# Kernel optimization log

Hardware: AMD Instinct MI355X
Metric: run time of the kernel (lower is better)

## Reference

```python
import jax, jax.numpy as jnp
import numpy as np

ALPHA = 0.25
GAMMA = 2.0
EPS = 1e-8


def _lsa(cost):
    """Jonker-Volgenant shortest-augmenting-path linear sum assignment.
    Matches scipy.optimize.linear_sum_assignment for rectangular matrices."""
    cost = np.asarray(cost, dtype=np.float64)
    transposed = cost.shape[0] > cost.shape[1]
    if transposed:
        cost = cost.T
    n, m = cost.shape  # n <= m
    INF = 1e18
    u = np.zeros(n + 1)
    v = np.zeros(m + 1)
    p = np.zeros(m + 1, dtype=np.int64)   # p[j] = row (1-indexed) assigned to col j
    way = np.zeros(m + 1, dtype=np.int64)
    for i in range(1, n + 1):
        p[0] = i
        j0 = 0
        minv = np.full(m + 1, INF)
        used = np.zeros(m + 1, dtype=bool)
        while True:
            used[j0] = True
            i0 = p[j0]
            cur = cost[i0 - 1] - u[i0] - v[1:]
            free = ~used[1:]
            better = free & (cur < minv[1:])
            minv[1:][better] = cur[better]
            way[1:][better] = j0
            masked = np.where(free, minv[1:], INF)
            j1 = int(np.argmin(masked)) + 1
            delta = masked[j1 - 1]
            u[p[used]] += delta
            v[used] -= delta
            minv[1:][free] -= delta
            j0 = j1
            if p[j0] == 0:
                break
        while j0 != 0:  # augment
            j1 = way[j0]
            p[j0] = p[j1]
            j0 = j1
    row_of_col = p[1:] - 1
    cols = np.nonzero(row_of_col >= 0)[0]
    rows = row_of_col[cols]
    if transposed:
        rows, cols = cols, rows
    order = np.argsort(rows)
    return rows[order], cols[order]


def _focal_cost(p):
    """pos_cost - neg_cost for sigmoid probs p, per focal-loss matcher cost."""
    neg = (1.0 - ALPHA) * p ** GAMMA * (-jnp.log(1.0 - p + EPS))
    pos = ALPHA * (1.0 - p) ** GAMMA * (-jnp.log(p + EPS))
    return pos - neg


def _match(rec, loc, targets):
    """rec: [bs, Q, Crec] logits; loc: [bs, Q, Cloc] logits; targets: [bs, nt] int.
    Returns (src_idx, tgt_idx) each [bs, nt] (query index, target index)."""
    nt = targets.shape[1]
    cost_class = jnp.take_along_axis(_focal_cost(jax.nn.sigmoid(rec)),
                                     targets[:, None, :], axis=2)      # [bs, Q, nt]
    cost_pos = _focal_cost(jax.nn.sigmoid(loc))[:, :, :nt]             # tgt_pos = arange(nt)
    C = np.asarray(2.0 * cost_class + cost_pos)                        # [bs, Q, nt]
    src, tgt = [], []
    for b in range(C.shape[0]):  # per-batch Hungarian, as in original
        r, c = _lsa(C[b])
        src.append(r)
        tgt.append(c)
    return jnp.asarray(np.stack(src)), jnp.asarray(np.stack(tgt))


def _ce(logits, labels):
    # F.cross_entropy with mean reduction
    logp = jax.nn.log_softmax(logits, axis=-1)
    return -jnp.mean(jnp.take_along_axis(logp, labels[..., None], axis=-1))


def setup_inputs() -> dict:
    key = jax.random.key(0)
    k1, k2, k3 = jax.random.split(key, 3)
    rec = jax.random.normal(k1, (128, 107, 32, 32), dtype=jnp.float32)
    loc = jax.random.normal(k2, (128, 25, 32, 32), dtype=jnp.float32)
    targets = jax.random.randint(k3, (128, 25), 0, 107, dtype=jnp.int64)
    return {"rec": rec, "loc": loc, "targets": targets}


def reference(rec, loc, targets):
    bs, c_rec, H, W = rec.shape
    c_loc = loc.shape[1]
    nt = targets.shape[1]
    rec = jnp.transpose(rec.reshape(bs, c_rec, H * W), (0, 2, 1))  # [bs, Q, Crec]
    loc = jnp.transpose(loc.reshape(bs, c_loc, H * W), (0, 2, 1))  # [bs, Q, Cloc]
    src_idx, tgt_idx = _match(rec, loc, targets)                   # [bs, nt] each
    rec_m = jnp.take_along_axis(rec, src_idx[:, :, None], axis=1)  # [bs, nt, Crec]
    loc_m = jnp.take_along_axis(loc, src_idx[:, :, None], axis=1)  # [bs, nt, Cloc]
    cls_labels = jnp.take_along_axis(targets, tgt_idx, axis=1)     # [bs, nt]
    pos_labels = tgt_idx                                           # tgt_pos[b, j] == j
    det_rec_losses = _ce(rec_m.reshape(bs * nt, c_rec), cls_labels.reshape(-1))
    pos_losses = _ce(loc_m.reshape(bs * nt, c_loc), pos_labels.reshape(-1))
    return (det_rec_losses, pos_losses)
```

## Files before the change

kernel.cpp:

```cpp
#include <hip/hip_runtime.h>
#include <hip/hip_bf16.h>
#include <math.h>

#define BS   128
#define NT   25
#define CREC 107
#define CLOC 25
#define QN   1024
#define INFD 1e18

__device__ __forceinline__ float focal_cost_f(float x) {
    float p   = 1.0f / (1.0f + __expf(-x));
    float neg = 0.75f * p * p * (-__logf(1.0f - p + 1e-8f));
    float pos = 0.25f * (1.0f - p) * (1.0f - p) * (-__logf(p + 1e-8f));
    return pos - neg;
}

__global__ __launch_bounds__(256)
void hungarian_kernel(const float* __restrict__ rec, const float* __restrict__ loc,
                      const int* __restrict__ targets, int* __restrict__ pairq_g) {
    const int b     = blockIdx.x;
    const int tid   = threadIdx.x;
    const int wave  = tid >> 6;
    const int lane  = tid & 63;
    const int qbase = (wave << 8) + (lane << 2);

    __shared__ int    way_s[QN + 1];
    __shared__ int    p_s[QN + 1];
    __shared__ double u_s[NT + 1];
    __shared__ int    t_s[NT];
    __shared__ float  bminv_s[NT][4];
    __shared__ int    bminq_s[NT][4];
    __shared__ float  rowmin_s[NT];
    __shared__ int    rowarg_s[NT];
    __shared__ int    unassigned_s[NT];
    __shared__ int    nun_s;
    __shared__ double candv_s[4];
    __shared__ int    candj_s[4];

    for (int j = tid; j <= QN; j += 256) { p_s[j] = 0; way_s[j] = 0; }
    if (tid < NT) t_s[tid] = targets[b * NT + tid];
    __syncthreads();

    const size_t rb0 = (size_t)b * CREC * QN;
    const size_t lb0 = (size_t)b * CLOC * QN;

    {
        float4 ra = *(const float4*)(rec + rb0 + (size_t)t_s[0] * QN + qbase);
        float4 la = *(const float4*)(loc + lb0 + qbase);
        for (int r = 0; r < NT; ++r) {
            float4 rn, ln;
            if (r + 1 < NT) {
                rn = *(const float4*)(rec + rb0 + (size_t)t_s[r + 1] * QN + qbase);
                ln = *(const float4*)(loc + lb0 + (size_t)(r + 1) * QN + qbase);
            }
            float c[4];
            c[0] = 2.0f * focal_cost_f(ra.x) + focal_cost_f(la.x);
            c[1] = 2.0f * focal_cost_f(ra.y) + focal_cost_f(la.y);
            c[2] = 2.0f * focal_cost_f(ra.z) + focal_cost_f(la.z);
            c[3] = 2.0f * focal_cost_f(ra.w) + focal_cost_f(la.w);
            float bv = c[0]; int bq = qbase;
            #pragma unroll
            for (int m = 1; m < 4; ++m)
                if (c[m] < bv) { bv = c[m]; bq = qbase + m; }
            #pragma unroll
            for (int off = 32; off; off >>= 1) {
                float ov = __shfl_xor(bv, off);
                int   oq = __shfl_xor(bq, off);
                if (ov < bv || (ov == bv && oq < bq)) { bv = ov; bq = oq; }
            }
            if (lane == 0) { bminv_s[r][wave] = bv; bminq_s[r][wave] = bq; }
            ra = rn; la = ln;
        }
    }
    __syncthreads();
    if (tid < NT) {
        float bv = bminv_s[tid][0]; int bq = bminq_s[tid][0];
        #pragma unroll
        for (int w = 1; w < 4; ++w) {
            float ov = bminv_s[tid][w]; int oq = bminq_s[tid][w];
            if (ov < bv || (ov == bv && oq < bq)) { bv = ov; bq = oq; }
        }
        rowmin_s[tid] = bv; rowarg_s[tid] = bq;
    }
    __syncthreads();
    if (tid == 0) {
        nun_s = 0;
        for (int r = 0; r < NT; ++r) {
            u_s[r + 1] = (double)rowmin_s[r];
            int j = rowarg_s[r] + 1;
            if (p_s[j] == 0) p_s[j] = r + 1;
            else             unassigned_s[nun_s++] = r + 1;
        }
    }
    __syncthreads();
    const int nun = nun_s;

    double v[4] = {0.0, 0.0, 0.0, 0.0};

    for (int s = 0; s < nun; ++s) {
        const int i = unassigned_s[s];
        double minv[4] = {INFD, INFD, INFD, INFD};
        unsigned usedmask = 0;
        int j0 = 0;

        for (;;) {
            int i0;
            if (j0 == 0) {
                i0 = i;
            } else {
                int q0 = j0 - 1;
                if ((q0 >> 2) == tid) {
                    int m = q0 & 3;
                    usedmask |= 1u << m;
                    minv[m] = INFD;
                }
                i0 = p_s[j0];
            }
            const double ui0 = u_s[i0];
            const float4 r4 = *(const float4*)(rec + rb0 + (size_t)t_s[i0 - 1] * QN + qbase);
            const float4 l4 = *(const float4*)(loc + lb0 + (size_t)(i0 - 1) * QN + qbase);
            float cf[4];
            cf[0] = 2.0f * focal_cost_f(r4.x) + focal_cost_f(l4.x);
            cf[1] = 2.0f * focal_cost_f(r4.y) + focal_cost_f(l4.y);
            cf[2] = 2.0f * focal_cost_f(r4.z) + focal_cost_f(l4.z);
            cf[3] = 2.0f * focal_cost_f(r4.w) + focal_cost_f(l4.w);

            double bestv = INFD; int bestj = QN + 2;
            #pragma unroll
            for (int m = 0; m < 4; ++m) {
                if (!(usedmask & (1u << m))) {
                    const int j = qbase + m + 1;
                    double cur = (double)cf[m] - ui0 - v[m];
                    if (cur < minv[m]) { minv[m] = cur; way_s[j] = j0; }
                    double mv = minv[m];
                    if (mv < bestv || (mv == bestv && j < bestj)) { bestv = mv; bestj = j; }
                }
            }
            #pragma unroll
            for (int off = 32; off; off >>= 1) {
                double ov = __shfl_xor(bestv, off);
                int    oj = __shfl_xor(bestj, off);
                if (ov < bestv || (ov == bestv && oj < bestj)) { bestv = ov; bestj = oj; }
            }
            if (lane == 0) { candv_s[wave] = bestv; candj_s[wave] = bestj; }
            __syncthreads();
            double delta = candv_s[0]; int j1 = candj_s[0];
            #pragma unroll
            for (int w = 1; w < 4; ++w) {
                double dv = candv_s[w]; int dj = candj_s[w];
                if (dv < delta || (dv == delta && dj < j1)) { delta = dv; j1 = dj; }
            }

            #pragma unroll
            for (int m = 0; m < 4; ++m) {
                if (usedmask & (1u << m)) v[m]    -= delta;
                else                      minv[m] -= delta;
            }
            if (tid == 0) u_s[i] += delta;
            unsigned mm = usedmask;
            while (mm) {
                int m = __ffs(mm) - 1; mm &= mm - 1;
                u_s[p_s[qbase + m + 1]] += delta;
            }
            __syncthreads();

            j0 = j1;
            if (p_s[j0] == 0) break;
        }
        if (tid == 0) {
            int jj = j0;
            while (jj != 0) {
                int jn = way_s[jj];
                p_s[jj] = (jn == 0) ? i : p_s[jn];
                jj = jn;
            }
        }
        __syncthreads();
    }

    for (int j = tid + 1; j <= QN; j += 256)
        if (p_s[j] > 0) pairq_g[b * NT + (p_s[j] - 1)] = j - 1;
}

__global__ __launch_bounds__(64)
void loss_kernel(const float* __restrict__ rec, const float* __restrict__ loc,
                 const int* __restrict__ targets, const int* __restrict__ pairq_g,
                 float* __restrict__ partial) {
    const int pid  = blockIdx.x;
    const int b    = pid / NT, t = pid % NT;
    const int lane = threadIdx.x;
    const int q    = pairq_g[pid];

    const float* rb = rec + (size_t)b * CREC * QN + q;
    float x0 = (lane < CREC)      ? rb[(size_t)lane * QN]        : -1e30f;
    float x1 = (lane + 64 < CREC) ? rb[(size_t)(lane + 64) * QN] : -1e30f;
    float mx = fmaxf(x0, x1);
    #pragma unroll
    for (int off = 32; off; off >>= 1) mx = fmaxf(mx, __shfl_xor(mx, off));
    float e = 0.0f;
    if (lane < CREC)      e += expf(x0 - mx);
    if (lane + 64 < CREC) e += expf(x1 - mx);
    #pragma unroll
    for (int off = 32; off; off >>= 1) e += __shfl_xor(e, off);
    float lse = mx + logf(e);

    const float* lb = loc + (size_t)b * CLOC * QN + q;
    float y = (lane < CLOC) ? lb[(size_t)lane * QN] : -1e30f;
    float my = y;
    #pragma unroll
    for (int off = 32; off; off >>= 1) my = fmaxf(my, __shfl_xor(my, off));
    float ey = (lane < CLOC) ? expf(y - my) : 0.0f;
    #pragma unroll
    for (int off = 32; off; off >>= 1) ey += __shfl_xor(ey, off);
    float lsey = my + logf(ey);

    if (lane == 0) {
        int lab = targets[pid];
        partial[pid]           = lse  - rb[(size_t)lab * QN];
        partial[BS * NT + pid] = lsey - lb[(size_t)t * QN];
    }
}

__global__ __launch_bounds__(256)
void finalize_kernel(const float* __restrict__ partial, float* __restrict__ out) {
    const int tid = threadIdx.x;
    float s0 = 0.0f, s1 = 0.0f;
    for (int i = tid; i < BS * NT; i += 256) {
        s0 += partial[i];
        s1 += partial[BS * NT + i];
    }
    __shared__ float a0[4], a1[4];
    #pragma unroll
    for (int off = 32; off; off >>= 1) { s0 += __shfl_xor(s0, off); s1 += __shfl_xor(s1, off); }
    if ((tid & 63) == 0) { a0[tid >> 6] = s0; a1[tid >> 6] = s1; }
    __syncthreads();
    if (tid == 0) {
        out[0] = (a0[0] + a0[1] + a0[2] + a0[3]) * (1.0f / (BS * NT));
        out[1] = (a1[0] + a1[1] + a1[2] + a1[3]) * (1.0f / (BS * NT));
    }
}

extern "C" void kernel_launch(void* const* d_in, const int* in_sizes, int n_in,
                              void* d_out, int out_size, void* d_ws, size_t ws_size,
                              hipStream_t stream) {
    (void)in_sizes; (void)n_in; (void)out_size; (void)ws_size;
    const float* rec     = (const float*)d_in[0];
    const float* loc     = (const float*)d_in[1];
    const int*   targets = (const int*)d_in[2];
    float* out = (float*)d_out;

    int*   pairq_g = (int*)d_ws;
    float* partial = (float*)(pairq_g + BS * NT);

    hipLaunchKernelGGL(hungarian_kernel, dim3(BS), dim3(256), 0, stream,
                       rec, loc, targets, pairq_g);
    hipLaunchKernelGGL(loss_kernel, dim3(BS * NT), dim3(64), 0, stream,
                       rec, loc, targets, pairq_g, partial);
    hipLaunchKernelGGL(finalize_kernel, dim3(1), dim3(256), 0, stream,
                       partial, out);
}
```

Measured before the change: 167.1 us.

## Split row-min init into parallel kernel and remove per-step barrier in Dijkstra loop

Moves the initial per-row minimum computation out of the per-batch Hungarian kernel into a separate kernel launched over batch×target blocks, so that work spreads across many more workgroups. Inside the augmenting search, the dual update of u is deferred to the end of each search using a running delta sum and per-column snapshots, and candidate slots are double-buffered by parity, which removes one __syncthreads per inner iteration. The way array is re-laid out with a padded stride to spread LDS banks. The cost is an extra launch, a global round trip for the row minima, and a little more register state per thread.

```diff
diff --git a/kernel.cpp b/kernel.cpp
--- a/kernel.cpp
+++ b/kernel.cpp
@@ -8,6 +8,11 @@
 #define CLOC 25
 #define QN   1024
 #define INFD 1e18
+#define WSTR 257
+__device__ __forceinline__ int widx(int j) {
+    int q = j - 1;
+    return (q & 3) * WSTR + (q >> 2);
+}
 
 __device__ __forceinline__ float focal_cost_f(float x) {
     float p   = 1.0f / (1.0f + __expf(-x));
@@ -17,73 +22,78 @@
 }
 
 __global__ __launch_bounds__(256)
-void hungarian_kernel(const float* __restrict__ rec, const float* __restrict__ loc,
-                      const int* __restrict__ targets, int* __restrict__ pairq_g) {
+void rowmin_kernel(const float* __restrict__ rec, const float* __restrict__ loc,
+                   const int* __restrict__ targets,
+                   float* __restrict__ rowmin_g, int* __restrict__ rowarg_g) {
+    const int pid   = blockIdx.x;
+    const int b     = pid / NT, r = pid % NT;
+    const int tid   = threadIdx.x;
+    const int qbase = tid << 2;
+    const int tc    = targets[pid];
+
+    float4 r4 = *(const float4*)(rec + ((size_t)b * CREC + tc) * QN + qbase);
+    float4 l4 = *(const float4*)(loc + ((size_t)b * CLOC + r)  * QN + qbase);
+    float c[4];
+    c[0] = 2.0f * focal_cost_f(r4.x) + focal_cost_f(l4.x);
+    c[1] = 2.0f * focal_cost_f(r4.y) + focal_cost_f(l4.y);
+    c[2] = 2.0f * focal_cost_f(r4.z) + focal_cost_f(l4.z);
+    c[3] = 2.0f * focal_cost_f(r4.w) + focal_cost_f(l4.w);
+
+    float bv = c[0]; int bq = qbase;
+    #pragma unroll
+    for (int m = 1; m < 4; ++m)
+        if (c[m] < bv) { bv = c[m]; bq = qbase + m; }
+    #pragma unroll
+    for (int off = 32; off; off >>= 1) {
+        float ov = __shfl_xor(bv, off);
+        int   oq = __shfl_xor(bq, off);
+        if (ov < bv || (ov == bv && oq < bq)) { bv = ov; bq = oq; }
+    }
+    __shared__ float bmv[4];
+    __shared__ int   bmq[4];
+    if ((tid & 63) == 0) { bmv[tid >> 6] = bv; bmq[tid >> 6] = bq; }
+    __syncthreads();
+    if (tid == 0) {
+        float fv = bmv[0]; int fq = bmq[0];
+        #pragma unroll
+        for (int w = 1; w < 4; ++w) {
+            float ov = bmv[w]; int oq = bmq[w];
+            if (ov < fv || (ov == fv && oq < fq)) { fv = ov; fq = oq; }
+        }
+        rowmin_g[pid] = fv; rowarg_g[pid] = fq;
+    }
+}
+
+__global__ __launch_bounds__(256)
+void search_kernel(const float* __restrict__ rec, const float* __restrict__ loc,
+                   const int* __restrict__ targets,
+                   const float* __restrict__ rowmin_g, const int* __restrict__ rowarg_g,
+                   int* __restrict__ pairq_g) {
     const int b     = blockIdx.x;
     const int tid   = threadIdx.x;
     const int wave  = tid >> 6;
     const int lane  = tid & 63;
-    const int qbase = (wave << 8) + (lane << 2);
-
-    __shared__ int    way_s[QN + 1];
+    const int qbase = tid << 2;
+
+    __shared__ int    way_s[4 * WSTR];
     __shared__ int    p_s[QN + 1];
     __shared__ double u_s[NT + 1];
     __shared__ int    t_s[NT];
-    __shared__ float  bminv_s[NT][4];
-    __shared__ int    bminq_s[NT][4];
     __shared__ float  rowmin_s[NT];
     __shared__ int    rowarg_s[NT];
     __shared__ int    unassigned_s[NT];
     __shared__ int    nun_s;
-    __shared__ double candv_s[4];
-    __shared__ int    candj_s[4];
-
-    for (int j = tid; j <= QN; j += 256) { p_s[j] = 0; way_s[j] = 0; }
-    if (tid < NT) t_s[tid] = targets[b * NT + tid];
-    __syncthreads();
-
-    const size_t rb0 = (size_t)b * CREC * QN;
-    const size_t lb0 = (size_t)b * CLOC * QN;
-
-    {
-        float4 ra = *(const float4*)(rec + rb0 + (size_t)t_s[0] * QN + qbase);
-        float4 la = *(const float4*)(loc + lb0 + qbase);
-        for (int r = 0; r < NT; ++r) {
-            float4 rn, ln;
-            if (r + 1 < NT) {
-                rn = *(const float4*)(rec + rb0 + (size_t)t_s[r + 1] * QN + qbase);
-                ln = *(const float4*)(loc + lb0 + (size_t)(r + 1) * QN + qbase);
-            }
-            float c[4];
-            c[0] = 2.0f * focal_cost_f(ra.x) + focal_cost_f(la.x);
-            c[1] = 2.0f * focal_cost_f(ra.y) + focal_cost_f(la.y);
-            c[2] = 2.0f * focal_cost_f(ra.z) + focal_cost_f(la.z);
-            c[3] = 2.0f * focal_cost_f(ra.w) + focal_cost_f(la.w);
-            float bv = c[0]; int bq = qbase;
-            #pragma unroll
-            for (int m = 1; m < 4; ++m)
-                if (c[m] < bv) { bv = c[m]; bq = qbase + m; }
-            #pragma unroll
-            for (int off = 32; off; off >>= 1) {
-                float ov = __shfl_xor(bv, off);
-                int   oq = __shfl_xor(bq, off);
-                if (ov < bv || (ov == bv && oq < bq)) { bv = ov; bq = oq; }
-            }
-            if (lane == 0) { bminv_s[r][wave] = bv; bminq_s[r][wave] = bq; }
-            ra = rn; la = ln;
-        }
-    }
-    __syncthreads();
+    __shared__ double candv_s[2][4];
+    __shared__ int    candj_s[2][4];
+
+    for (int j = tid; j <= QN; j += 256) p_s[j] = 0;
     if (tid < NT) {
-        float bv = bminv_s[tid][0]; int bq = bminq_s[tid][0];
-        #pragma unroll
-        for (int w = 1; w < 4; ++w) {
-            float ov = bminv_s[tid][w]; int oq = bminq_s[tid][w];
-            if (ov < bv || (ov == bv && oq < bq)) { bv = ov; bq = oq; }
-        }
-        rowmin_s[tid] = bv; rowarg_s[tid] = bq;
-    }
-    __syncthreads();
+        t_s[tid]      = targets[b * NT + tid];
+        rowmin_s[tid] = rowmin_g[b * NT + tid];
+        rowarg_s[tid] = rowarg_g[b * NT + tid];
+    }
+    __syncthreads();
+
     if (tid == 0) {
         nun_s = 0;
         for (int r = 0; r < NT; ++r) {
@@ -96,13 +106,19 @@
     __syncthreads();
     const int nun = nun_s;
 
+    const size_t rb0 = (size_t)b * CREC * QN;
+    const size_t lb0 = (size_t)b * CLOC * QN;
+
     double v[4] = {0.0, 0.0, 0.0, 0.0};
 
     for (int s = 0; s < nun; ++s) {
         const int i = unassigned_s[s];
         double minv[4] = {INFD, INFD, INFD, INFD};
+        double snap[4] = {0.0, 0.0, 0.0, 0.0};
+        double dsum    = 0.0;
         unsigned usedmask = 0;
         int j0 = 0;
+        int parity = 0;
 
         for (;;) {
             int i0;
@@ -114,6 +130,7 @@
                     int m = q0 & 3;
                     usedmask |= 1u << m;
                     minv[m] = INFD;
+                    snap[m] = dsum;
                 }
                 i0 = p_s[j0];
             }
@@ -132,7 +149,7 @@
                 if (!(usedmask & (1u << m))) {
                     const int j = qbase + m + 1;
                     double cur = (double)cf[m] - ui0 - v[m];
-                    if (cur < minv[m]) { minv[m] = cur; way_s[j] = j0; }
+                    if (cur < minv[m]) { minv[m] = cur; way_s[widx(j)] = j0; }
                     double mv = minv[m];
                     if (mv < bestv || (mv == bestv && j < bestj)) { bestv = mv; bestj = j; }
                 }
@@ -143,35 +160,37 @@
                 int    oj = __shfl_xor(bestj, off);
                 if (ov < bestv || (ov == bestv && oj < bestj)) { bestv = ov; bestj = oj; }
             }
-            if (lane == 0) { candv_s[wave] = bestv; candj_s[wave] = bestj; }
+            if (lane == 0) { candv_s[parity][wave] = bestv; candj_s[parity][wave] = bestj; }
             __syncthreads();
-            double delta = candv_s[0]; int j1 = candj_s[0];
+            double delta = candv_s[parity][0]; int j1 = candj_s[parity][0];
             #pragma unroll
             for (int w = 1; w < 4; ++w) {
-                double dv = candv_s[w]; int dj = candj_s[w];
+                double dv = candv_s[parity][w]; int dj = candj_s[parity][w];
                 if (dv < delta || (dv == delta && dj < j1)) { delta = dv; j1 = dj; }
             }
+            parity ^= 1;
+            dsum += delta;
 
             #pragma unroll
             for (int m = 0; m < 4; ++m) {
                 if (usedmask & (1u << m)) v[m]    -= delta;
                 else                      minv[m] -= delta;
             }
-            if (tid == 0) u_s[i] += delta;
-            unsigned mm = usedmask;
-            while (mm) {
-                int m = __ffs(mm) - 1; mm &= mm - 1;
-                u_s[p_s[qbase + m + 1]] += delta;
-            }
-            __syncthreads();
-
             j0 = j1;
             if (p_s[j0] == 0) break;
         }
+
+        if (tid == 0) u_s[i] += dsum;
+        unsigned mm = usedmask;
+        while (mm) {
+            int m = __ffs(mm) - 1; mm &= mm - 1;
+            u_s[p_s[qbase + m + 1]] += dsum - snap[m];
+        }
+        __syncthreads();
         if (tid == 0) {
             int jj = j0;
             while (jj != 0) {
-                int jn = way_s[jj];
+                int jn = way_s[widx(jj)];
                 p_s[jj] = (jn == 0) ? i : p_s[jn];
                 jj = jn;
             }
@@ -250,11 +269,15 @@
     const int*   targets = (const int*)d_in[2];
     float* out = (float*)d_out;
 
-    int*   pairq_g = (int*)d_ws;
-    float* partial = (float*)(pairq_g + BS * NT);
-
-    hipLaunchKernelGGL(hungarian_kernel, dim3(BS), dim3(256), 0, stream,
-                       rec, loc, targets, pairq_g);
+    float* rowmin_g = (float*)d_ws;
+    int*   rowarg_g = (int*)(rowmin_g + BS * NT);
+    int*   pairq_g  = (int*)(rowarg_g + BS * NT);
+    float* partial  = (float*)(pairq_g + BS * NT);
+
+    hipLaunchKernelGGL(rowmin_kernel, dim3(BS * NT), dim3(256), 0, stream,
+                       rec, loc, targets, rowmin_g, rowarg_g);
+    hipLaunchKernelGGL(search_kernel, dim3(BS), dim3(256), 0, stream,
+                       rec, loc, targets, rowmin_g, rowarg_g, pairq_g);
     hipLaunchKernelGGL(loss_kernel, dim3(BS * NT), dim3(64), 0, stream,
                        rec, loc, targets, pairq_g, partial);
     hipLaunchKernelGGL(finalize_kernel, dim3(1), dim3(256), 0, stream,
```

Measured after the change: 155.3 us. 1.08x faster.

## Cache focal cost tile in LDS and defer dual updates to one barrier

Applied to the files above, without the earlier changes.

Computes the 25x1024 cost matrix once per batch into dynamic shared memory (100 KB), so each Dijkstra step reads costs from LDS instead of reloading global memory and recomputing transcendentals. Row dual updates for used columns are deferred with per-column delta snapshots and applied once after the search. This drops one of the two barriers per inner iteration; the candidate buffer is double-buffered by parity to stay safe. The way array is re-laid out with a padded stride to avoid LDS bank conflicts. The large LDS footprint limits blocks per CU, but the grid is only 128 blocks.

```diff
diff --git a/kernel.cpp b/kernel.cpp
--- a/kernel.cpp
+++ b/kernel.cpp
@@ -8,6 +8,11 @@
 #define CLOC 25
 #define QN   1024
 #define INFD 1e18
+#define WSTR 257
+__device__ __forceinline__ int widx(int j) {
+    int q = j - 1;
+    return (q & 3) * WSTR + (q >> 2);
+}
 
 __device__ __forceinline__ float focal_cost_f(float x) {
     float p   = 1.0f / (1.0f + __expf(-x));
@@ -17,28 +22,29 @@
 }
 
 __global__ __launch_bounds__(256)
-void hungarian_kernel(const float* __restrict__ rec, const float* __restrict__ loc,
-                      const int* __restrict__ targets, int* __restrict__ pairq_g) {
+void search_kernel(const float* __restrict__ rec, const float* __restrict__ loc,
+                   const int* __restrict__ targets, int* __restrict__ pairq_g) {
+    extern __shared__ float cost_s[];
     const int b     = blockIdx.x;
     const int tid   = threadIdx.x;
     const int wave  = tid >> 6;
     const int lane  = tid & 63;
-    const int qbase = (wave << 8) + (lane << 2);
-
-    __shared__ int    way_s[QN + 1];
+    const int qbase = tid << 2;
+
+    __shared__ int    way_s[3 * WSTR + 256];
     __shared__ int    p_s[QN + 1];
     __shared__ double u_s[NT + 1];
     __shared__ int    t_s[NT];
-    __shared__ float  bminv_s[NT][4];
-    __shared__ int    bminq_s[NT][4];
+    __shared__ float  bmv_s[NT][4];
+    __shared__ int    bmq_s[NT][4];
     __shared__ float  rowmin_s[NT];
     __shared__ int    rowarg_s[NT];
     __shared__ int    unassigned_s[NT];
     __shared__ int    nun_s;
-    __shared__ double candv_s[4];
-    __shared__ int    candj_s[4];
-
-    for (int j = tid; j <= QN; j += 256) { p_s[j] = 0; way_s[j] = 0; }
+    __shared__ double candv_s[2][4];
+    __shared__ int    candj_s[2][4];
+
+    for (int j = tid; j <= QN; j += 256) p_s[j] = 0;
     if (tid < NT) t_s[tid] = targets[b * NT + tid];
     __syncthreads();
 
@@ -54,31 +60,37 @@
                 rn = *(const float4*)(rec + rb0 + (size_t)t_s[r + 1] * QN + qbase);
                 ln = *(const float4*)(loc + lb0 + (size_t)(r + 1) * QN + qbase);
             }
-            float c[4];
-            c[0] = 2.0f * focal_cost_f(ra.x) + focal_cost_f(la.x);
-            c[1] = 2.0f * focal_cost_f(ra.y) + focal_cost_f(la.y);
-            c[2] = 2.0f * focal_cost_f(ra.z) + focal_cost_f(la.z);
-            c[3] = 2.0f * focal_cost_f(ra.w) + focal_cost_f(la.w);
-            float bv = c[0]; int bq = qbase;
-            #pragma unroll
-            for (int m = 1; m < 4; ++m)
-                if (c[m] < bv) { bv = c[m]; bq = qbase + m; }
-            #pragma unroll
-            for (int off = 32; off; off >>= 1) {
-                float ov = __shfl_xor(bv, off);
-                int   oq = __shfl_xor(bq, off);
-                if (ov < bv || (ov == bv && oq < bq)) { bv = ov; bq = oq; }
-            }
-            if (lane == 0) { bminv_s[r][wave] = bv; bminq_s[r][wave] = bq; }
-            ra = rn; la = ln;
-        }
+            float4 c;
+            c.x = 2.0f * focal_cost_f(ra.x) + focal_cost_f(la.x);
+            c.y = 2.0f * focal_cost_f(ra.y) + focal_cost_f(la.y);
+            c.z = 2.0f * focal_cost_f(ra.z) + focal_cost_f(la.z);
+            c.w = 2.0f * focal_cost_f(ra.w) + focal_cost_f(la.w);
+            *(float4*)(cost_s + (r << 10) + qbase) = c;
+            if (r + 1 < NT) { ra = rn; la = ln; }
+        }
+    }
+    __syncthreads();
+
+    for (int r = 0; r < NT; ++r) {
+        float4 c = *(const float4*)(cost_s + (r << 10) + qbase);
+        float bv = c.x; int bq = qbase;
+        if (c.y < bv) { bv = c.y; bq = qbase + 1; }
+        if (c.z < bv) { bv = c.z; bq = qbase + 2; }
+        if (c.w < bv) { bv = c.w; bq = qbase + 3; }
+        #pragma unroll
+        for (int off = 32; off; off >>= 1) {
+            float ov = __shfl_xor(bv, off);
+            int   oq = __shfl_xor(bq, off);
+            if (ov < bv || (ov == bv && oq < bq)) { bv = ov; bq = oq; }
+        }
+        if (lane == 0) { bmv_s[r][wave] = bv; bmq_s[r][wave] = bq; }
     }
     __syncthreads();
     if (tid < NT) {
-        float bv = bminv_s[tid][0]; int bq = bminq_s[tid][0];
+        float bv = bmv_s[tid][0]; int bq = bmq_s[tid][0];
         #pragma unroll
         for (int w = 1; w < 4; ++w) {
-            float ov = bminv_s[tid][w]; int oq = bminq_s[tid][w];
+            float ov = bmv_s[tid][w]; int oq = bmq_s[tid][w];
             if (ov < bv || (ov == bv && oq < bq)) { bv = ov; bq = oq; }
         }
         rowmin_s[tid] = bv; rowarg_s[tid] = bq;
@@ -101,8 +113,11 @@
     for (int s = 0; s < nun; ++s) {
         const int i = unassigned_s[s];
         double minv[4] = {INFD, INFD, INFD, INFD};
+        double snap[4] = {0.0, 0.0, 0.0, 0.0};
+        double dsum    = 0.0;
         unsigned usedmask = 0;
         int j0 = 0;
+        int parity = 0;
 
         for (;;) {
             int i0;
@@ -114,17 +129,13 @@
                     int m = q0 & 3;
                     usedmask |= 1u << m;
                     minv[m] = INFD;
+                    snap[m] = dsum;
                 }
                 i0 = p_s[j0];
             }
             const double ui0 = u_s[i0];
-            const float4 r4 = *(const float4*)(rec + rb0 + (size_t)t_s[i0 - 1] * QN + qbase);
-            const float4 l4 = *(const float4*)(loc + lb0 + (size_t)(i0 - 1) * QN + qbase);
-            float cf[4];
-            cf[0] = 2.0f * focal_cost_f(r4.x) + focal_cost_f(l4.x);
-            cf[1] = 2.0f * focal_cost_f(r4.y) + focal_cost_f(l4.y);
-            cf[2] = 2.0f * focal_cost_f(r4.z) + focal_cost_f(l4.z);
-            cf[3] = 2.0f * focal_cost_f(r4.w) + focal_cost_f(l4.w);
+            const float4 c4 = *(const float4*)(cost_s + ((i0 - 1) << 10) + qbase);
+            const float cf[4] = { c4.x, c4.y, c4.z, c4.w };
 
             double bestv = INFD; int bestj = QN + 2;
             #pragma unroll
@@ -132,7 +143,7 @@
                 if (!(usedmask & (1u << m))) {
                     const int j = qbase + m + 1;
                     double cur = (double)cf[m] - ui0 - v[m];
-                    if (cur < minv[m]) { minv[m] = cur; way_s[j] = j0; }
+                    if (cur < minv[m]) { minv[m] = cur; way_s[widx(j)] = j0; }
                     double mv = minv[m];
                     if (mv < bestv || (mv == bestv && j < bestj)) { bestv = mv; bestj = j; }
                 }
@@ -143,35 +154,37 @@
                 int    oj = __shfl_xor(bestj, off);
                 if (ov < bestv || (ov == bestv && oj < bestj)) { bestv = ov; bestj = oj; }
             }
-            if (lane == 0) { candv_s[wave] = bestv; candj_s[wave] = bestj; }
+            if (lane == 0) { candv_s[parity][wave] = bestv; candj_s[parity][wave] = bestj; }
             __syncthreads();
-            double delta = candv_s[0]; int j1 = candj_s[0];
+            double delta = candv_s[parity][0]; int j1 = candj_s[parity][0];
             #pragma unroll
             for (int w = 1; w < 4; ++w) {
-                double dv = candv_s[w]; int dj = candj_s[w];
+                double dv = candv_s[parity][w]; int dj = candj_s[parity][w];
                 if (dv < delta || (dv == delta && dj < j1)) { delta = dv; j1 = dj; }
             }
+            parity ^= 1;
+            dsum += delta;
 
             #pragma unroll
             for (int m = 0; m < 4; ++m) {
                 if (usedmask & (1u << m)) v[m]    -= delta;
                 else                      minv[m] -= delta;
             }
-            if (tid == 0) u_s[i] += delta;
-            unsigned mm = usedmask;
-            while (mm) {
-                int m = __ffs(mm) - 1; mm &= mm - 1;
-                u_s[p_s[qbase + m + 1]] += delta;
-            }
-            __syncthreads();
-
             j0 = j1;
             if (p_s[j0] == 0) break;
         }
+
+        if (tid == 0) u_s[i] += dsum;
+        unsigned mm = usedmask;
+        while (mm) {
+            int m = __ffs(mm) - 1; mm &= mm - 1;
+            u_s[p_s[qbase + m + 1]] += dsum - snap[m];
+        }
+        __syncthreads();
         if (tid == 0) {
             int jj = j0;
             while (jj != 0) {
-                int jn = way_s[jj];
+                int jn = way_s[widx(jj)];
                 p_s[jj] = (jn == 0) ? i : p_s[jn];
                 jj = jn;
             }
@@ -253,7 +266,11 @@
     int*   pairq_g = (int*)d_ws;
     float* partial = (float*)(pairq_g + BS * NT);
 
-    hipLaunchKernelGGL(hungarian_kernel, dim3(BS), dim3(256), 0, stream,
+    const int tile_bytes = NT * QN * (int)sizeof(float);
+    (void)hipFuncSetAttribute((const void*)search_kernel,
+                              hipFuncAttributeMaxDynamicSharedMemorySize, tile_bytes);
+
+    hipLaunchKernelGGL(search_kernel, dim3(BS), dim3(256), tile_bytes, stream,
                        rec, loc, targets, pairq_g);
     hipLaunchKernelGGL(loss_kernel, dim3(BS * NT), dim3(64), 0, stream,
                        rec, loc, targets, pairq_g, partial);
```

Result: no change. 167.5 us (+0.3%).
